# Kernel tuning notes

Measured on AMD Instinct MI355X. Metric: run time of the kernel, lower is better.

Reference implementation:

```python
import jax, jax.numpy as jnp
import numpy as np

N_NODES = 20000   # max_childs
N_EDGES = 640000
FEAT = 256        # node_feat_size
HID = 128         # node_hidden_size
NUM_SEM = 57
EDGE_TYPES = 4
EDGE_FEAT = 8


def setup_inputs() -> dict:
    key = jax.random.key(0)
    ks = jax.random.split(key, 10)
    inp = {
        "child_feats": jax.random.normal(ks[0], (1, N_NODES, FEAT + NUM_SEM), jnp.float32),
        "child_exists": jnp.ones((1, N_NODES, 1), jnp.float32),
        "edge_type_onehot": jax.random.uniform(ks[1], (1, N_EDGES, EDGE_TYPES), jnp.float32),
        "edge_feats": jax.random.normal(ks[2], (1, N_EDGES, EDGE_FEAT), jnp.float32),
        "edge_indices": jax.random.randint(ks[3], (1, N_EDGES, 2), 0, N_NODES, jnp.int64 if jax.config.jax_enable_x64 else jnp.int32),
        "W_child": jax.random.normal(ks[4], (FEAT + NUM_SEM, HID), jnp.float32) * 0.05,
        "b_child": jnp.zeros((HID,), jnp.float32),
        "W_edge0": jax.random.normal(ks[5], (2 * HID + EDGE_FEAT + EDGE_TYPES, HID), jnp.float32) * 0.05,
        "b_edge0": jnp.zeros((HID,), jnp.float32),
        "W_edge1": jax.random.normal(ks[6], (2 * HID + EDGE_FEAT + EDGE_TYPES, HID), jnp.float32) * 0.05,
        "b_edge1": jnp.zeros((HID,), jnp.float32),
        "W_parent": jax.random.normal(ks[7], (3 * HID, FEAT), jnp.float32) * 0.05,
        "b_parent": jnp.zeros((FEAT,), jnp.float32),
    }
    return inp


def reference(child_feats, child_exists, edge_type_onehot, edge_feats, edge_indices,
              W_child, b_child, W_edge0, b_edge0, W_edge1, b_edge1, W_parent, b_parent):
    # child_op + existence mask: [1, N, FEAT+NUM_SEM] -> [N, HID]
    h = jax.nn.relu(child_feats @ W_child + b_child) * child_exists
    h = h[0]  # batch_size is hard-coded to 1 in the original module

    # symmetric_type == 'max': pool over children
    iter_parent_feats = [jnp.max(h, axis=0)]

    # edge features: cat(edge_type_onehot, edge_feats) -> [E, ET+EF]
    ef = jnp.concatenate([edge_type_onehot[0], edge_feats[0]], axis=1)
    src = edge_indices[0, :, 0]
    dst = edge_indices[0, :, 1]

    for W, b in ((W_edge0, b_edge0), (W_edge1, b_edge1)):
        # gather -> per-edge MLP: [E, 2*HID + ET + EF] -> [E, HID]
        msg = jax.nn.relu(jnp.concatenate([h[src], h[dst], ef], axis=1) @ W + b)
        # edge_symmetric_type == 'max' with zero-initialized out buffer:
        # result = max(0, segment_max(msg)) per node
        h = jnp.maximum(jax.ops.segment_max(msg, src, num_segments=N_NODES), 0.0)
        iter_parent_feats.append(jnp.max(h, axis=0))

    parent = jnp.concatenate(iter_parent_feats)[None, :]  # [1, 3*HID]
    return jax.nn.relu(parent @ W_parent + b_parent)       # [1, FEAT]
```

## Files before the change

kernel.cpp:

```cpp
#include <hip/hip_runtime.h>

#define N_NODES   20000
#define N_EDGES   640000
#define CF        313
#define KC        320
#define ROWB      640

typedef __attribute__((ext_vector_type(8))) short short8;
typedef __attribute__((ext_vector_type(4))) float f32x4;
typedef __attribute__((ext_vector_type(4))) unsigned short u16x4;

static __device__ __forceinline__ unsigned short f2bf(float f) {
    unsigned u = __float_as_uint(f);
    u = u + 0x7FFFu + ((u >> 16) & 1u);
    return (unsigned short)(u >> 16);
}
static __device__ __forceinline__ float bflo(unsigned u) { return __uint_as_float(u << 16); }
static __device__ __forceinline__ float bfhi(unsigned u) { return __uint_as_float(u & 0xffff0000u); }
static __device__ __forceinline__ int pkbf(float a, float b) {
    return (int)((unsigned)f2bf(a) | ((unsigned)f2bf(b) << 16));
}

__global__ void prep_weights(const float* __restrict__ Wc,
                             const float* __restrict__ We0,
                             const float* __restrict__ We1,
                             unsigned short* __restrict__ WcT,
                             unsigned short* __restrict__ Wab0,
                             unsigned short* __restrict__ Wab1) {
    int g = blockIdx.x * 256 + threadIdx.x;
    if (g < 128 * KC) {
        int n = g / KC, k = g % KC;
        WcT[g] = f2bf(k < CF ? Wc[k * 128 + n] : 0.f);
    } else if (g < 128 * KC + 32768) {
        int h = g - 128 * KC;
        int n = h >> 7, k = h & 127;
        Wab0[h] = f2bf(n < 128 ? We0[k * 128 + n] : We0[(128 + k) * 128 + (n - 128)]);
    } else {
        int h = g - 128 * KC - 32768;
        int n = h >> 7, k = h & 127;
        Wab1[h] = f2bf(n < 128 ? We1[k * 128 + n] : We1[(128 + k) * 128 + (n - 128)]);
    }
}

__global__ void hist_kernel(const int* __restrict__ eidx, unsigned* __restrict__ hist) {
    int e = blockIdx.x * 256 + threadIdx.x;
    if (e < N_EDGES) atomicAdd(hist + eidx[2 * e], 1u);
}

__global__ void scan_kernel(const unsigned* __restrict__ hist,
                            unsigned* __restrict__ cursor,
                            unsigned* __restrict__ cstart) {
    __shared__ unsigned part[1024];
    int t = threadIdx.x;
    unsigned loc[20];
    unsigned s = 0;
    int base = t * 20;
    if (t < 1000) {
        #pragma unroll
        for (int i = 0; i < 20; ++i) { loc[i] = hist[base + i]; s += loc[i]; }
    }
    part[t] = s;
    __syncthreads();
    for (int off = 1; off < 1024; off <<= 1) {
        unsigned u = (t >= off) ? part[t - off] : 0u;
        __syncthreads();
        part[t] += u;
        __syncthreads();
    }
    if (t < 1000) {
        unsigned run = part[t] - s;
        #pragma unroll
        for (int i = 0; i < 20; ++i) {
            cursor[base + i] = run;
            cstart[base + i] = run;
            run += loc[i];
        }
    }
}

__global__ void scatter_kernel(const int* __restrict__ eidx,
                               const float* __restrict__ onehot,
                               const float* __restrict__ efeat,
                               unsigned* __restrict__ cursor,
                               int4* __restrict__ es) {
    int e = blockIdx.x * 256 + threadIdx.x;
    if (e >= N_EDGES) return;
    int2 sd = ((const int2*)eidx)[e];
    unsigned pos = atomicAdd(cursor + sd.x, 1u);
    float4 oh = *(const float4*)(onehot + 4 * (size_t)e);
    float4 ea = *(const float4*)(efeat + 8 * (size_t)e);
    float4 eb = *(const float4*)(efeat + 8 * (size_t)e + 4);
    int4 w0, w1;
    w0.x = sd.y;
    w0.y = pkbf(oh.x, oh.y); w0.z = pkbf(oh.z, oh.w); w0.w = pkbf(ea.x, ea.y);
    w1.x = pkbf(ea.z, ea.w); w1.y = pkbf(eb.x, eb.y); w1.z = pkbf(eb.z, eb.w); w1.w = 0;
    es[2 * (size_t)pos]     = w0;
    es[2 * (size_t)pos + 1] = w1;
}

__global__ __launch_bounds__(256, 2)
void child_gemm(const float* __restrict__ cf,
                const float* __restrict__ exists,
                const unsigned short* __restrict__ WT,
                const float* __restrict__ bias,
                unsigned short* __restrict__ hbf,
                unsigned int* __restrict__ pmax) {
    __shared__ __align__(16) unsigned char Alds[64 * ROWB];

    const int tid  = threadIdx.x;
    const int lane = tid & 63;
    const int wave = tid >> 6;
    const int n0   = wave * 32;
    const int row0 = blockIdx.x * 64;

    short8 bfrag[10][2];
    {
        int col  = n0 + (lane & 15);
        int krow = (lane >> 4) * 8;
        #pragma unroll
        for (int ks = 0; ks < 10; ++ks)
            #pragma unroll
            for (int nt = 0; nt < 2; ++nt)
                bfrag[ks][nt] = *(const short8*)(WT + (col + nt * 16) * KC + ks * 32 + krow);
    }
    float bv[2];
    bv[0] = bias[n0 + (lane & 15)];
    bv[1] = bias[n0 + 16 + (lane & 15)];

    {
        int r = tid >> 2, p = tid & 3;
        int node = row0 + r;
        bool valid = node < N_NODES;
        const float* g = cf + (size_t)node * CF;
        unsigned rbase = r * ROWB;
        unsigned sw = (r & 7) << 4;
        #pragma unroll
        for (int i = 0; i < 10; ++i) {
            int c = p + i * 4;
            short8 v = {};
            if (valid) {
                #pragma unroll
                for (int kk = 0; kk < 8; ++kk) {
                    int k = c * 8 + kk;
                    if (k < CF) v[kk] = (short)f2bf(g[k]);
                }
            }
            *(short8*)(Alds + ((rbase + c * 16) ^ sw)) = v;
        }
    }
    __syncthreads();

    f32x4 acc[4][2] = {};
    {
        int arow = lane & 15;
        unsigned kb = (lane >> 4) * 16;
        #pragma unroll
        for (int ks = 0; ks < 10; ++ks)
            #pragma unroll
            for (int mt = 0; mt < 4; ++mt) {
                int row = mt * 16 + arow;
                short8 a = *(const short8*)(Alds + (((unsigned)row * ROWB + ks * 64 + kb) ^ ((row & 7) << 4)));
                acc[mt][0] = __builtin_amdgcn_mfma_f32_16x16x32_bf16(a, bfrag[ks][0], acc[mt][0], 0, 0, 0);
                acc[mt][1] = __builtin_amdgcn_mfma_f32_16x16x32_bf16(a, bfrag[ks][1], acc[mt][1], 0, 0, 0);
            }
    }

    {
        int rb = (lane >> 4) * 4;
        #pragma unroll
        for (int nt = 0; nt < 2; ++nt) {
            int col = n0 + nt * 16 + (lane & 15);
            float m = 0.f;
            #pragma unroll
            for (int mt = 0; mt < 4; ++mt)
                #pragma unroll
                for (int j = 0; j < 4; ++j) {
                    int node = row0 + mt * 16 + rb + j;
                    float v = 0.f;
                    if (node < N_NODES) {
                        v = fmaxf(acc[mt][nt][j] + bv[nt], 0.f) * exists[node];
                        hbf[node * 128 + col] = f2bf(v);
                    }
                    m = fmaxf(m, v);
                }
            m = fmaxf(m, __shfl_xor(m, 16));
            m = fmaxf(m, __shfl_xor(m, 32));
            if ((lane >> 4) == 0)
                atomicMax(pmax + col, __float_as_uint(m));
        }
    }
}

__global__ __launch_bounds__(256)
void gemmAB(const unsigned short* __restrict__ hbf,
            const unsigned short* __restrict__ WT,
            const float* __restrict__ bias,
            float* __restrict__ Afl,
            unsigned short* __restrict__ Bbf) {
    const int tid  = threadIdx.x;
    const int lane = tid & 63;
    const int wave = tid >> 6;
    const int n0   = wave * 64;
    const int row0 = blockIdx.x * 64;
    const int krow = (lane >> 4) * 8;

    short8 bfrag[4][4];
    {
        int colb = n0 + (lane & 15);
        #pragma unroll
        for (int ks = 0; ks < 4; ++ks)
            #pragma unroll
            for (int nt = 0; nt < 4; ++nt)
                bfrag[ks][nt] = *(const short8*)(WT + (colb + nt * 16) * 128 + ks * 32 + krow);
    }

    f32x4 acc[4][4] = {};
    #pragma unroll
    for (int ks = 0; ks < 4; ++ks)
        #pragma unroll
        for (int mt = 0; mt < 4; ++mt) {
            int row = row0 + mt * 16 + (lane & 15);
            row = min(row, N_NODES - 1);
            short8 a = *(const short8*)(hbf + (size_t)row * 128 + ks * 32 + krow);
            #pragma unroll
            for (int nt = 0; nt < 4; ++nt)
                acc[mt][nt] = __builtin_amdgcn_mfma_f32_16x16x32_bf16(a, bfrag[ks][nt], acc[mt][nt], 0, 0, 0);
        }

    {
        int rb = (lane >> 4) * 4;
        #pragma unroll
        for (int nt = 0; nt < 4; ++nt) {
            int col = n0 + nt * 16 + (lane & 15);
            float badd = (col < 128) ? bias[col] : 0.f;
            #pragma unroll
            for (int mt = 0; mt < 4; ++mt)
                #pragma unroll
                for (int j = 0; j < 4; ++j) {
                    int row = row0 + mt * 16 + rb + j;
                    if (row < N_NODES) {
                        float v = acc[mt][nt][j] + badd;
                        if (col < 128) Afl[(size_t)row * 128 + col] = v;
                        else           Bbf[(size_t)row * 128 + col - 128] = f2bf(v);
                    }
                }
        }
    }
}

__global__ __launch_bounds__(512)
void edge_pass(const unsigned short* __restrict__ Bbf,
               const float* __restrict__ Afl,
               const int4* __restrict__ es,
               const float* __restrict__ Wef,
               const unsigned* __restrict__ cstart,
               const unsigned* __restrict__ hist,
               unsigned short* __restrict__ hbf,
               unsigned* __restrict__ pslice) {
    __shared__ unsigned cmax[128];
    const int tid = threadIdx.x;
    if (tid < 128) cmax[tid] = 0;
    __syncthreads();

    const int s  = blockIdx.x * 16 + (tid >> 5);
    const int c0 = (tid & 31) * 4;

    float4 wf[12];
    #pragma unroll
    for (int k = 0; k < 12; ++k) wf[k] = *(const float4*)(Wef + k * 128 + c0);

    float m0 = -1e30f, m1 = -1e30f, m2 = -1e30f, m3 = -1e30f;
    const unsigned cnt = hist[s];
    if (cnt) {
        const int4* p = es + 2 * (size_t)cstart[s];
        const unsigned last = cnt - 1;
        int4 ra0 = p[0], rb0 = p[1];
        unsigned j1 = min(1u, last), j2 = min(2u, last);
        int4 ra1 = p[2 * j1], rb1 = p[2 * j1 + 1];
        int4 ra2 = p[2 * j2], rb2 = p[2 * j2 + 1];
        u16x4 b0 = *(const u16x4*)(Bbf + (size_t)(unsigned)ra0.x * 128 + c0);
        u16x4 b1 = *(const u16x4*)(Bbf + (size_t)(unsigned)ra1.x * 128 + c0);
        #pragma unroll 4
        for (unsigned i = 0; i < cnt; ++i) {
            u16x4 b2 = *(const u16x4*)(Bbf + (size_t)(unsigned)ra2.x * 128 + c0);
            unsigned j3 = min(i + 3, last);
            int4 ra3 = p[2 * j3], rb3 = p[2 * j3 + 1];

            float ef[12];
            unsigned u;
            u = (unsigned)ra0.y; ef[0] = bflo(u);  ef[1] = bfhi(u);
            u = (unsigned)ra0.z; ef[2] = bflo(u);  ef[3] = bfhi(u);
            u = (unsigned)ra0.w; ef[4] = bflo(u);  ef[5] = bfhi(u);
            u = (unsigned)rb0.x; ef[6] = bflo(u);  ef[7] = bfhi(u);
            u = (unsigned)rb0.y; ef[8] = bflo(u);  ef[9] = bfhi(u);
            u = (unsigned)rb0.z; ef[10] = bflo(u); ef[11] = bfhi(u);

            float x0 = bflo((unsigned)(unsigned short)b0[0] << 0 | 0u), x1, x2, x3;
            x0 = __uint_as_float(((unsigned)(unsigned short)b0[0]) << 16);
            x1 = __uint_as_float(((unsigned)(unsigned short)b0[1]) << 16);
            x2 = __uint_as_float(((unsigned)(unsigned short)b0[2]) << 16);
            x3 = __uint_as_float(((unsigned)(unsigned short)b0[3]) << 16);
            #pragma unroll
            for (int k = 0; k < 12; ++k) {
                x0 = fmaf(ef[k], wf[k].x, x0);
                x1 = fmaf(ef[k], wf[k].y, x1);
                x2 = fmaf(ef[k], wf[k].z, x2);
                x3 = fmaf(ef[k], wf[k].w, x3);
            }
            m0 = fmaxf(m0, x0); m1 = fmaxf(m1, x1);
            m2 = fmaxf(m2, x2); m3 = fmaxf(m3, x3);

            ra0 = ra1; rb0 = rb1; ra1 = ra2; rb1 = rb2; ra2 = ra3; rb2 = rb3;
            b0 = b1; b1 = b2;
        }
    }

    float4 a = *(const float4*)(Afl + (size_t)s * 128 + c0);
    float h0 = fmaxf(a.x + m0, 0.f), h1 = fmaxf(a.y + m1, 0.f);
    float h2 = fmaxf(a.z + m2, 0.f), h3 = fmaxf(a.w + m3, 0.f);

    unsigned lo = (unsigned)f2bf(h0) | ((unsigned)f2bf(h1) << 16);
    unsigned hi = (unsigned)f2bf(h2) | ((unsigned)f2bf(h3) << 16);
    *(uint2*)(hbf + (size_t)s * 128 + c0) = make_uint2(lo, hi);

    float g0 = fmaxf(h0, __shfl_xor(h0, 32));
    float g1 = fmaxf(h1, __shfl_xor(h1, 32));
    float g2 = fmaxf(h2, __shfl_xor(h2, 32));
    float g3 = fmaxf(h3, __shfl_xor(h3, 32));
    if ((tid & 63) < 32) {
        atomicMax(&cmax[c0],     __float_as_uint(g0));
        atomicMax(&cmax[c0 + 1], __float_as_uint(g1));
        atomicMax(&cmax[c0 + 2], __float_as_uint(g2));
        atomicMax(&cmax[c0 + 3], __float_as_uint(g3));
    }
    __syncthreads();
    if (tid < 128) atomicMax(pslice + tid, cmax[tid]);
}

__global__ void final_gemm(const float* __restrict__ parent,
                           const float* __restrict__ Wp,
                           const float* __restrict__ bp,
                           float* __restrict__ out) {
    __shared__ float p[384];
    int t = threadIdx.x;
    for (int i = t; i < 384; i += 256) p[i] = parent[i];
    __syncthreads();
    float s = bp[t];
    for (int k = 0; k < 384; ++k) s += p[k] * Wp[k * 256 + t];
    out[t] = fmaxf(s, 0.f);
}

extern "C" void kernel_launch(void* const* d_in, const int* in_sizes, int n_in,
                              void* d_out, int out_size, void* d_ws, size_t ws_size,
                              hipStream_t stream) {
    const float* child_feats  = (const float*)d_in[0];
    const float* child_exists = (const float*)d_in[1];
    const float* onehot       = (const float*)d_in[2];
    const float* efeat        = (const float*)d_in[3];
    const int*   eidx         = (const int*)d_in[4];
    const float* Wc  = (const float*)d_in[5];
    const float* bc  = (const float*)d_in[6];
    const float* We0 = (const float*)d_in[7];
    const float* be0 = (const float*)d_in[8];
    const float* We1 = (const float*)d_in[9];
    const float* be1 = (const float*)d_in[10];
    const float* Wp  = (const float*)d_in[11];
    const float* bp  = (const float*)d_in[12];

    char* ws = (char*)d_ws;
    unsigned short* hbf    = (unsigned short*)(ws);
    float*          Afl    = (float*)(ws + 5120000);
    unsigned short* Bbf    = (unsigned short*)(ws + 15360000);
    int4*           es     = (int4*)(ws + 20480000);
    unsigned short* WcT    = (unsigned short*)(ws + 40960000);
    unsigned short* Wab0   = (unsigned short*)(ws + 41041920);
    unsigned short* Wab1   = (unsigned short*)(ws + 41107456);
    unsigned*       parent = (unsigned*)(ws + 41172992);
    unsigned*       hist   = (unsigned*)(ws + 41174528);
    unsigned*       cstart = (unsigned*)(ws + 41254528);
    unsigned*       cursor = (unsigned*)(ws + 41334528);

    const float* Wef0 = We0 + 256 * 128;
    const float* Wef1 = We1 + 256 * 128;

    hipMemsetAsync(parent, 0, 384 * 4, stream);
    hipMemsetAsync(hist, 0, N_NODES * 4, stream);

    prep_weights<<<416, 256, 0, stream>>>(Wc, We0, We1, WcT, Wab0, Wab1);
    hist_kernel<<<2500, 256, 0, stream>>>(eidx, hist);
    scan_kernel<<<1, 1024, 0, stream>>>(hist, cursor, cstart);
    scatter_kernel<<<2500, 256, 0, stream>>>(eidx, onehot, efeat, cursor, es);

    child_gemm<<<313, 256, 0, stream>>>(child_feats, child_exists, WcT, bc, hbf, parent);

    gemmAB<<<313, 256, 0, stream>>>(hbf, Wab0, be0, Afl, Bbf);
    edge_pass<<<1250, 512, 0, stream>>>(Bbf, Afl, es, Wef0, cstart, hist, hbf, parent + 128);

    gemmAB<<<313, 256, 0, stream>>>(hbf, Wab1, be1, Afl, Bbf);
    edge_pass<<<1250, 512, 0, stream>>>(Bbf, Afl, es, Wef1, cstart, hist, hbf, parent + 256);

    final_gemm<<<1, 256, 0, stream>>>((const float*)parent, Wp, bp, (float*)d_out);
}
```

Baseline: 324.4 us.

## Merge setup kernels, pre-convert child features, use fp16 dot2 in edge pass

Fuses weight prep, the edge histogram and a new child-feature bf16 conversion pass into one setup launch. child_gemm now reads the pre-packed bf16 rows instead of converting fp32 on the fly. Edge features are packed as fp16 and the per-edge 12-term MLP uses fdot2 with a deeper prefetch, and edge_pass uses 256-thread blocks. final_gemm splits K across 1024 threads. In exchange it adds an extra write and read of a 12.8 MB buffer and lowers edge feature precision to fp16.

```diff
diff --git a/kernel.cpp b/kernel.cpp
--- a/kernel.cpp
+++ b/kernel.cpp
@@ -9,42 +9,64 @@
 typedef __attribute__((ext_vector_type(8))) short short8;
 typedef __attribute__((ext_vector_type(4))) float f32x4;
 typedef __attribute__((ext_vector_type(4))) unsigned short u16x4;
+typedef _Float16 h2 __attribute__((ext_vector_type(2)));
 
 static __device__ __forceinline__ unsigned short f2bf(float f) {
     unsigned u = __float_as_uint(f);
     u = u + 0x7FFFu + ((u >> 16) & 1u);
     return (unsigned short)(u >> 16);
 }
-static __device__ __forceinline__ float bflo(unsigned u) { return __uint_as_float(u << 16); }
-static __device__ __forceinline__ float bfhi(unsigned u) { return __uint_as_float(u & 0xffff0000u); }
-static __device__ __forceinline__ int pkbf(float a, float b) {
-    return (int)((unsigned)f2bf(a) | ((unsigned)f2bf(b) << 16));
-}
-
-__global__ void prep_weights(const float* __restrict__ Wc,
+static __device__ __forceinline__ int pkh(float a, float b) {
+    h2 h; h.x = (_Float16)a; h.y = (_Float16)b;
+    return __builtin_bit_cast(int, h);
+}
+static __device__ __forceinline__ h2 bch(int v) { return __builtin_bit_cast(h2, v); }
+static __device__ __forceinline__ float dot2f(h2 a, h2 b, float c) {
+    return __builtin_amdgcn_fdot2(a, b, c, false);
+}
+
+__global__ void setup_kernel(const float* __restrict__ Wc,
                              const float* __restrict__ We0,
                              const float* __restrict__ We1,
+                             const int* __restrict__ eidx,
+                             const float* __restrict__ cf,
                              unsigned short* __restrict__ WcT,
                              unsigned short* __restrict__ Wab0,
-                             unsigned short* __restrict__ Wab1) {
-    int g = blockIdx.x * 256 + threadIdx.x;
-    if (g < 128 * KC) {
-        int n = g / KC, k = g % KC;
-        WcT[g] = f2bf(k < CF ? Wc[k * 128 + n] : 0.f);
-    } else if (g < 128 * KC + 32768) {
-        int h = g - 128 * KC;
-        int n = h >> 7, k = h & 127;
-        Wab0[h] = f2bf(n < 128 ? We0[k * 128 + n] : We0[(128 + k) * 128 + (n - 128)]);
+                             unsigned short* __restrict__ Wab1,
+                             unsigned* __restrict__ hist,
+                             unsigned short* __restrict__ cfp) {
+    const int b = blockIdx.x, tid = threadIdx.x;
+    if (b < 416) {
+        int g = b * 256 + tid;
+        if (g < 128 * KC) {
+            int n = g / KC, k = g % KC;
+            WcT[g] = f2bf(k < CF ? Wc[k * 128 + n] : 0.f);
+        } else if (g < 128 * KC + 32768) {
+            int h = g - 128 * KC;
+            int n = h >> 7, k = h & 127;
+            Wab0[h] = f2bf(n < 128 ? We0[k * 128 + n] : We0[(128 + k) * 128 + (n - 128)]);
+        } else {
+            int h = g - 128 * KC - 32768;
+            int n = h >> 7, k = h & 127;
+            Wab1[h] = f2bf(n < 128 ? We1[k * 128 + n] : We1[(128 + k) * 128 + (n - 128)]);
+        }
+    } else if (b < 2916) {
+        int e = (b - 416) * 256 + tid;
+        if (e < N_EDGES) atomicAdd(hist + eidx[2 * e], 1u);
     } else {
-        int h = g - 128 * KC - 32768;
-        int n = h >> 7, k = h & 127;
-        Wab1[h] = f2bf(n < 128 ? We1[k * 128 + n] : We1[(128 + k) * 128 + (n - 128)]);
-    }
-}
-
-__global__ void hist_kernel(const int* __restrict__ eidx, unsigned* __restrict__ hist) {
-    int e = blockIdx.x * 256 + threadIdx.x;
-    if (e < N_EDGES) atomicAdd(hist + eidx[2 * e], 1u);
+        int g = (b - 2916) * 256 + tid;
+        if (g < 800000) {
+            int node = g / 40, c = g - node * 40;
+            const float* base = cf + (size_t)node * CF;
+            short8 v = {};
+            #pragma unroll
+            for (int kk = 0; kk < 8; ++kk) {
+                int k = c * 8 + kk;
+                if (k < CF) v[kk] = (short)f2bf(base[k]);
+            }
+            *(short8*)(cfp + (size_t)g * 8) = v;
+        }
+    }
 }
 
 __global__ void scan_kernel(const unsigned* __restrict__ hist,
@@ -92,14 +114,14 @@
     float4 eb = *(const float4*)(efeat + 8 * (size_t)e + 4);
     int4 w0, w1;
     w0.x = sd.y;
-    w0.y = pkbf(oh.x, oh.y); w0.z = pkbf(oh.z, oh.w); w0.w = pkbf(ea.x, ea.y);
-    w1.x = pkbf(ea.z, ea.w); w1.y = pkbf(eb.x, eb.y); w1.z = pkbf(eb.z, eb.w); w1.w = 0;
+    w0.y = pkh(oh.x, oh.y); w0.z = pkh(oh.z, oh.w); w0.w = pkh(ea.x, ea.y);
+    w1.x = pkh(ea.z, ea.w); w1.y = pkh(eb.x, eb.y); w1.z = pkh(eb.z, eb.w); w1.w = 0;
     es[2 * (size_t)pos]     = w0;
     es[2 * (size_t)pos + 1] = w1;
 }
 
 __global__ __launch_bounds__(256, 2)
-void child_gemm(const float* __restrict__ cf,
+void child_gemm(const unsigned short* __restrict__ cfp,
                 const float* __restrict__ exists,
                 const unsigned short* __restrict__ WT,
                 const float* __restrict__ bias,
@@ -131,20 +153,13 @@
         int r = tid >> 2, p = tid & 3;
         int node = row0 + r;
         bool valid = node < N_NODES;
-        const float* g = cf + (size_t)node * CF;
         unsigned rbase = r * ROWB;
         unsigned sw = (r & 7) << 4;
         #pragma unroll
         for (int i = 0; i < 10; ++i) {
             int c = p + i * 4;
             short8 v = {};
-            if (valid) {
-                #pragma unroll
-                for (int kk = 0; kk < 8; ++kk) {
-                    int k = c * 8 + kk;
-                    if (k < CF) v[kk] = (short)f2bf(g[k]);
-                }
-            }
+            if (valid) v = *(const short8*)(cfp + (size_t)node * KC + c * 8);
             *(short8*)(Alds + ((rbase + c * 16) ^ sw)) = v;
         }
     }
@@ -248,7 +263,7 @@
     }
 }
 
-__global__ __launch_bounds__(512)
+__global__ __launch_bounds__(256)
 void edge_pass(const unsigned short* __restrict__ Bbf,
                const float* __restrict__ Afl,
                const int4* __restrict__ es,
@@ -262,70 +277,78 @@
     if (tid < 128) cmax[tid] = 0;
     __syncthreads();
 
-    const int s  = blockIdx.x * 16 + (tid >> 5);
+    const int s  = blockIdx.x * 8 + (tid >> 5);
     const int c0 = (tid & 31) * 4;
 
-    float4 wf[12];
+    h2 wf[6][4];
     #pragma unroll
-    for (int k = 0; k < 12; ++k) wf[k] = *(const float4*)(Wef + k * 128 + c0);
+    for (int kp = 0; kp < 6; ++kp)
+        #pragma unroll
+        for (int j = 0; j < 4; ++j) {
+            h2 w;
+            w.x = (_Float16)Wef[(2 * kp) * 128 + c0 + j];
+            w.y = (_Float16)Wef[(2 * kp + 1) * 128 + c0 + j];
+            wf[kp][j] = w;
+        }
 
     float m0 = -1e30f, m1 = -1e30f, m2 = -1e30f, m3 = -1e30f;
     const unsigned cnt = hist[s];
     if (cnt) {
         const int4* p = es + 2 * (size_t)cstart[s];
         const unsigned last = cnt - 1;
-        int4 ra0 = p[0], rb0 = p[1];
-        unsigned j1 = min(1u, last), j2 = min(2u, last);
+        unsigned j1 = min(1u, last), j2 = min(2u, last), j3 = min(3u, last);
+        int4 ra0 = p[0],      rb0 = p[1];
         int4 ra1 = p[2 * j1], rb1 = p[2 * j1 + 1];
         int4 ra2 = p[2 * j2], rb2 = p[2 * j2 + 1];
+        int4 ra3 = p[2 * j3], rb3 = p[2 * j3 + 1];
         u16x4 b0 = *(const u16x4*)(Bbf + (size_t)(unsigned)ra0.x * 128 + c0);
         u16x4 b1 = *(const u16x4*)(Bbf + (size_t)(unsigned)ra1.x * 128 + c0);
+        u16x4 b2 = *(const u16x4*)(Bbf + (size_t)(unsigned)ra2.x * 128 + c0);
         #pragma unroll 4
         for (unsigned i = 0; i < cnt; ++i) {
-            u16x4 b2 = *(const u16x4*)(Bbf + (size_t)(unsigned)ra2.x * 128 + c0);
-            unsigned j3 = min(i + 3, last);
-            int4 ra3 = p[2 * j3], rb3 = p[2 * j3 + 1];
-
-            float ef[12];
-            unsigned u;
-            u = (unsigned)ra0.y; ef[0] = bflo(u);  ef[1] = bfhi(u);
-            u = (unsigned)ra0.z; ef[2] = bflo(u);  ef[3] = bfhi(u);
-            u = (unsigned)ra0.w; ef[4] = bflo(u);  ef[5] = bfhi(u);
-            u = (unsigned)rb0.x; ef[6] = bflo(u);  ef[7] = bfhi(u);
-            u = (unsigned)rb0.y; ef[8] = bflo(u);  ef[9] = bfhi(u);
-            u = (unsigned)rb0.z; ef[10] = bflo(u); ef[11] = bfhi(u);
-
-            float x0 = bflo((unsigned)(unsigned short)b0[0] << 0 | 0u), x1, x2, x3;
-            x0 = __uint_as_float(((unsigned)(unsigned short)b0[0]) << 16);
-            x1 = __uint_as_float(((unsigned)(unsigned short)b0[1]) << 16);
-            x2 = __uint_as_float(((unsigned)(unsigned short)b0[2]) << 16);
-            x3 = __uint_as_float(((unsigned)(unsigned short)b0[3]) << 16);
-            #pragma unroll
-            for (int k = 0; k < 12; ++k) {
-                x0 = fmaf(ef[k], wf[k].x, x0);
-                x1 = fmaf(ef[k], wf[k].y, x1);
-                x2 = fmaf(ef[k], wf[k].z, x2);
-                x3 = fmaf(ef[k], wf[k].w, x3);
-            }
+            u16x4 b3 = *(const u16x4*)(Bbf + (size_t)(unsigned)ra3.x * 128 + c0);
+            unsigned j4 = min(i + 4, last);
+            int4 ra4 = p[2 * j4], rb4 = p[2 * j4 + 1];
+
+            h2 e0 = bch(ra0.y), e1 = bch(ra0.z), e2 = bch(ra0.w);
+            h2 e3 = bch(rb0.x), e4 = bch(rb0.y), e5 = bch(rb0.z);
+
+            float x0 = __uint_as_float(((unsigned)(unsigned short)b0[0]) << 16);
+            float x1 = __uint_as_float(((unsigned)(unsigned short)b0[1]) << 16);
+            float x2 = __uint_as_float(((unsigned)(unsigned short)b0[2]) << 16);
+            float x3 = __uint_as_float(((unsigned)(unsigned short)b0[3]) << 16);
+            x0 = dot2f(e0, wf[0][0], x0); x1 = dot2f(e0, wf[0][1], x1);
+            x2 = dot2f(e0, wf[0][2], x2); x3 = dot2f(e0, wf[0][3], x3);
+            x0 = dot2f(e1, wf[1][0], x0); x1 = dot2f(e1, wf[1][1], x1);
+            x2 = dot2f(e1, wf[1][2], x2); x3 = dot2f(e1, wf[1][3], x3);
+            x0 = dot2f(e2, wf[2][0], x0); x1 = dot2f(e2, wf[2][1], x1);
+            x2 = dot2f(e2, wf[2][2], x2); x3 = dot2f(e2, wf[2][3], x3);
+            x0 = dot2f(e3, wf[3][0], x0); x1 = dot2f(e3, wf[3][1], x1);
+            x2 = dot2f(e3, wf[3][2], x2); x3 = dot2f(e3, wf[3][3], x3);
+            x0 = dot2f(e4, wf[4][0], x0); x1 = dot2f(e4, wf[4][1], x1);
+            x2 = dot2f(e4, wf[4][2], x2); x3 = dot2f(e4, wf[4][3], x3);
+            x0 = dot2f(e5, wf[5][0], x0); x1 = dot2f(e5, wf[5][1], x1);
+            x2 = dot2f(e5, wf[5][2], x2); x3 = dot2f(e5, wf[5][3], x3);
             m0 = fmaxf(m0, x0); m1 = fmaxf(m1, x1);
             m2 = fmaxf(m2, x2); m3 = fmaxf(m3, x3);
 
-            ra0 = ra1; rb0 = rb1; ra1 = ra2; rb1 = rb2; ra2 = ra3; rb2 = rb3;
-            b0 = b1; b1 = b2;
+            ra0 = ra1; rb0 = rb1; ra1 = ra2; rb1 = rb2;
+            ra2 = ra3; rb2 = rb3; ra3 = ra4; rb3 = rb4;
+            b0 = b1; b1 = b2; b2 = b3;
         }
     }
 
     float4 a = *(const float4*)(Afl + (size_t)s * 128 + c0);
     float h0 = fmaxf(a.x + m0, 0.f), h1 = fmaxf(a.y + m1, 0.f);
-    float h2 = fmaxf(a.z + m2, 0.f), h3 = fmaxf(a.w + m3, 0.f);
+    float h2v = fmaxf(a.z + m2, 0.f), h3 = fmaxf(a.w + m3, 0.f);
 
     unsigned lo = (unsigned)f2bf(h0) | ((unsigned)f2bf(h1) << 16);
-    unsigned hi = (unsigned)f2bf(h2) | ((unsigned)f2bf(h3) << 16);
+    unsigned hi = (unsigned)f2bf(h2v) | ((unsigned)f2bf(h3) << 16);
     *(uint2*)(hbf + (size_t)s * 128 + c0) = make_uint2(lo, hi);
 
     float g0 = fmaxf(h0, __shfl_xor(h0, 32));
     float g1 = fmaxf(h1, __shfl_xor(h1, 32));
-    float g2 = fmaxf(h2, __shfl_xor(h2, 32));
+    float g2 = fmaxf(h2v, __shfl_xor(h2v, 32));
     float g3 = fmaxf(h3, __shfl_xor(h3, 32));
     if ((tid & 63) < 32) {
         atomicMax(&cmax[c0],     __float_as_uint(g0));
@@ -342,12 +365,17 @@
                            const float* __restrict__ bp,
                            float* __restrict__ out) {
     __shared__ float p[384];
+    __shared__ float red[1024];
     int t = threadIdx.x;
-    for (int i = t; i < 384; i += 256) p[i] = parent[i];
-    __syncthreads();
-    float s = bp[t];
-    for (int k = 0; k < 384; ++k) s += p[k] * Wp[k * 256 + t];
-    out[t] = fmaxf(s, 0.f);
+    if (t < 384) p[t] = parent[t];
+    __syncthreads();
+    int col = t & 255, kc = t >> 8;
+    float s = 0.f;
+    for (int k = kc * 96; k < kc * 96 + 96; ++k) s += p[k] * Wp[k * 256 + col];
+    red[t] = s;
+    __syncthreads();
+    if (kc == 0)
+        out[col] = fmaxf(red[col] + red[col + 256] + red[col + 512] + red[col + 768] + bp[col], 0.f);
 }
 
 extern "C" void kernel_launch(void* const* d_in, const int* in_sizes, int n_in,
@@ -372,13 +400,14 @@
     float*          Afl    = (float*)(ws + 5120000);
     unsigned short* Bbf    = (unsigned short*)(ws + 15360000);
     int4*           es     = (int4*)(ws + 20480000);
-    unsigned short* WcT    = (unsigned short*)(ws + 40960000);
-    unsigned short* Wab0   = (unsigned short*)(ws + 41041920);
-    unsigned short* Wab1   = (unsigned short*)(ws + 41107456);
-    unsigned*       parent = (unsigned*)(ws + 41172992);
-    unsigned*       hist   = (unsigned*)(ws + 41174528);
-    unsigned*       cstart = (unsigned*)(ws + 41254528);
-    unsigned*       cursor = (unsigned*)(ws + 41334528);
+    unsigned short* cfp    = (unsigned short*)(ws + 40960000);
+    unsigned short* WcT    = (unsigned short*)(ws + 53760000);
+    unsigned short* Wab0   = (unsigned short*)(ws + 53841920);
+    unsigned short* Wab1   = (unsigned short*)(ws + 53907456);
+    unsigned*       parent = (unsigned*)(ws + 53972992);
+    unsigned*       hist   = (unsigned*)(ws + 53974528);
+    unsigned*       cstart = (unsigned*)(ws + 54054528);
+    unsigned*       cursor = (unsigned*)(ws + 54134528);
 
     const float* Wef0 = We0 + 256 * 128;
     const float* Wef1 = We1 + 256 * 128;
@@ -386,18 +415,17 @@
     hipMemsetAsync(parent, 0, 384 * 4, stream);
     hipMemsetAsync(hist, 0, N_NODES * 4, stream);
 
-    prep_weights<<<416, 256, 0, stream>>>(Wc, We0, We1, WcT, Wab0, Wab1);
-    hist_kernel<<<2500, 256, 0, stream>>>(eidx, hist);
+    setup_kernel<<<6041, 256, 0, stream>>>(Wc, We0, We1, eidx, child_feats,
+                                           WcT, Wab0, Wab1, hist, cfp);
     scan_kernel<<<1, 1024, 0, stream>>>(hist, cursor, cstart);
+    child_gemm<<<313, 256, 0, stream>>>(cfp, child_exists, WcT, bc, hbf, parent);
     scatter_kernel<<<2500, 256, 0, stream>>>(eidx, onehot, efeat, cursor, es);
 
-    child_gemm<<<313, 256, 0, stream>>>(child_feats, child_exists, WcT, bc, hbf, parent);
-
     gemmAB<<<313, 256, 0, stream>>>(hbf, Wab0, be0, Afl, Bbf);
-    edge_pass<<<1250, 512, 0, stream>>>(Bbf, Afl, es, Wef0, cstart, hist, hbf, parent + 128);
+    edge_pass<<<2500, 256, 0, stream>>>(Bbf, Afl, es, Wef0, cstart, hist, hbf, parent + 128);
 
     gemmAB<<<313, 256, 0, stream>>>(hbf, Wab1, be1, Afl, Bbf);
-    edge_pass<<<1250, 512, 0, stream>>>(Bbf, Afl, es, Wef1, cstart, hist, hbf, parent + 256);
-
-    final_gemm<<<1, 256, 0, stream>>>((const float*)parent, Wp, bp, (float*)d_out);
-}
+    edge_pass<<<2500, 256, 0, stream>>>(Bbf, Afl, es, Wef1, cstart, hist, hbf, parent + 256);
+
+    final_gemm<<<1, 1024, 0, stream>>>((const float*)parent, Wp, bp, (float*)d_out);
+}
```

Measured after the change: 295.4 us. -8.9%, faster.
